# Performance work log

Hardware: AMD Instinct MI355X
Metric: run time of the kernel (lower is better)

## Reference

```python
import jax, jax.numpy as jnp
import numpy as np

B, T, D = 32, 2048, 256   # batch, encoder time steps, input_dim
H = 256                   # output_dim (GRU hidden)
A = 128                   # attention_dim
C = 4367                  # nb_classes
STEPS = 22                # max_out_t_steps


def setup_inputs() -> dict:
    key = jax.random.key(0)
    ks = jax.random.split(key, 11)
    s = 0.05
    return {
        "x": jax.random.normal(ks[0], (B, T, D), dtype=jnp.float32),
        # additive attention params: softmax_T(tanh(x Wx + h Wh) @ v)
        "Wx": jax.random.normal(ks[1], (D, A), dtype=jnp.float32) * s,
        "Wh": jax.random.normal(ks[2], (H, A), dtype=jnp.float32) * s,
        "v": jax.random.normal(ks[3], (A,), dtype=jnp.float32) * s,
        # torch GRUCell params
        "W_ih": jax.random.normal(ks[4], (3 * H, D), dtype=jnp.float32) * s,
        "W_hh": jax.random.normal(ks[5], (3 * H, H), dtype=jnp.float32) * s,
        "b_ih": jax.random.normal(ks[6], (3 * H,), dtype=jnp.float32) * s,
        "b_hh": jax.random.normal(ks[7], (3 * H,), dtype=jnp.float32) * s,
        # classifier
        "W_cls": jax.random.normal(ks[8], (C, H), dtype=jnp.float32) * s,
        "b_cls": jax.random.normal(ks[9], (C,), dtype=jnp.float32) * s,
    }


def reference(x, Wx, Wh, v, W_ih, W_hh, b_ih, b_hh, W_cls, b_cls):
    # dropout layers are identity in eval/reference mode
    xW = jnp.einsum("btd,da->bta", x, Wx)  # hoisted: constant across steps
    h0 = jnp.zeros((x.shape[0], H), dtype=x.dtype)

    def step(h, _):
        # additive attention over time axis
        e = jnp.einsum("bta,a->bt", jnp.tanh(xW + (h @ Wh)[:, None, :]), v)
        att = jax.nn.softmax(e, axis=1)          # [B, T]
        ctx = jnp.einsum("btd,bt->bd", x, att)   # weighted sum over T
        # torch GRUCell
        gi = ctx @ W_ih.T + b_ih                  # [B, 3H]
        gh = h @ W_hh.T + b_hh                    # [B, 3H]
        i_r, i_z, i_n = jnp.split(gi, 3, axis=1)
        h_r, h_z, h_n = jnp.split(gh, 3, axis=1)
        r = jax.nn.sigmoid(i_r + h_r)
        z = jax.nn.sigmoid(i_z + h_z)
        n = jnp.tanh(i_n + r * h_n)
        h_new = (1.0 - z) * n + z * h
        logits = h_new @ W_cls.T + b_cls          # [B, C]
        return h_new, logits

    _, outs = jax.lax.scan(step, h0, None, length=STEPS)  # [STEPS, B, C]
    return jnp.transpose(outs, (1, 0, 2))                 # [B, STEPS, C]
```

## Files before the change

kernel.cpp:

```cpp
#include <hip/hip_runtime.h>

#define BB 32
#define TT 2048
#define DD 256
#define HH 256
#define AA 128
#define CC 4367
#define CLS_LD 4480
#define NSTEPS 22
#define NCHUNK 32

typedef unsigned short ushortT;
typedef unsigned int uintT;
using frag8 = __attribute__((ext_vector_type(8))) short;
using f32x4 = __attribute__((ext_vector_type(4))) float;

__device__ __forceinline__ float tanh_fast(float u) {
  float e = __expf(2.0f * u);
  return 1.0f - 2.0f / (e + 1.0f);
}
__device__ __forceinline__ float sigmoid_fast(float u) {
  return 1.0f / (1.0f + __expf(-u));
}
__device__ __forceinline__ ushortT f2bf(float f) {
  unsigned int u = __float_as_uint(f);
  unsigned int r = (u + 0x7FFFu + ((u >> 16) & 1u)) >> 16;
  return (ushortT)r;
}
__device__ __forceinline__ float bf2f(ushortT v) {
  return __uint_as_float(((unsigned int)v) << 16);
}

__global__ __launch_bounds__(256) void trans_kernel(
    const float* __restrict__ Wx, const float* __restrict__ W_cls,
    float* __restrict__ WclsT, ushortT* __restrict__ WxT_bf) {
  int blk = blockIdx.x;
  __shared__ float tile[32][33];
  const int li = threadIdx.x >> 5, lj = threadIdx.x & 31;
  if (blk < 1096) {
    int i0 = (blk >> 3) * 32, j0 = (blk & 7) * 32;
#pragma unroll
    for (int k = 0; k < 4; ++k) {
      int i = i0 + li + k * 8;
      if (i < CC) tile[li + k * 8][lj] = W_cls[(size_t)i * 256 + j0 + lj];
    }
    __syncthreads();
#pragma unroll
    for (int k = 0; k < 4; ++k) {
      int j = j0 + li + k * 8, i = i0 + lj;
      if (i < CC) WclsT[(size_t)j * CLS_LD + i] = tile[lj][li + k * 8];
    }
  } else {
    blk -= 1096;
    int i0 = (blk >> 2) * 32, j0 = (blk & 3) * 32;
#pragma unroll
    for (int k = 0; k < 4; ++k)
      tile[li + k * 8][lj] = Wx[(size_t)(i0 + li + k * 8) * 128 + j0 + lj];
    __syncthreads();
#pragma unroll
    for (int k = 0; k < 4; ++k) {
      int j = j0 + li + k * 8;
      WxT_bf[(size_t)j * 256 + i0 + lj] = f2bf(tile[lj][li + k * 8]);
    }
  }
}

__global__ __launch_bounds__(256) void xw_mfma(
    const float* __restrict__ x, const ushortT* __restrict__ WxT_bf,
    ushortT* __restrict__ x_bf, ushortT* __restrict__ xWT) {
  __shared__ ushortT lds[2 * 128 * 72];
#define SX(r, c) lds[(r) * 72 + (c)]
#define SW(r, c) lds[128 * 72 + (r) * 72 + (c)]
#define ST(a, m) lds[(a) * 136 + (m)]
  const int tid = threadIdx.x;
  const int lane = tid & 63, w = tid >> 6;
  const int l15 = lane & 15, quad = lane >> 4;
  const int r0 = blockIdx.x * 128;
  const int bb = blockIdx.x >> 4, t0 = (blockIdx.x & 15) * 128;
  const int row = tid >> 1, half = tid & 1;

  f32x4 acc[2][8];
#pragma unroll
  for (int mt = 0; mt < 2; ++mt)
#pragma unroll
    for (int nt = 0; nt < 8; ++nt) acc[mt][nt] = (f32x4){0.f, 0.f, 0.f, 0.f};

  for (int kk0 = 0; kk0 < 256; kk0 += 64) {
    {
      const float4* xp = (const float4*)(x + (size_t)(r0 + row) * DD + kk0 + half * 32);
      uint4 pk[4];
#pragma unroll
      for (int i = 0; i < 4; ++i) {
        float4 f0 = xp[2 * i], f1 = xp[2 * i + 1];
        pk[i].x = (uintT)f2bf(f0.x) | ((uintT)f2bf(f0.y) << 16);
        pk[i].y = (uintT)f2bf(f0.z) | ((uintT)f2bf(f0.w) << 16);
        pk[i].z = (uintT)f2bf(f1.x) | ((uintT)f2bf(f1.y) << 16);
        pk[i].w = (uintT)f2bf(f1.z) | ((uintT)f2bf(f1.w) << 16);
      }
      uint4* sxp = (uint4*)&SX(row, half * 32);
      uint4* gxp = (uint4*)(x_bf + (size_t)(r0 + row) * DD + kk0 + half * 32);
#pragma unroll
      for (int i = 0; i < 4; ++i) { sxp[i] = pk[i]; gxp[i] = pk[i]; }
    }
    {
      const uint4* wp = (const uint4*)(WxT_bf + (size_t)row * DD + kk0 + half * 32);
      uint4* swp = (uint4*)&SW(row, half * 32);
#pragma unroll
      for (int i = 0; i < 4; ++i) swp[i] = wp[i];
    }
    __syncthreads();
#pragma unroll
    for (int kk = 0; kk < 2; ++kk) {
      frag8 a0 = *(const frag8*)&SX(w * 32 + l15, kk * 32 + quad * 8);
      frag8 a1 = *(const frag8*)&SX(w * 32 + 16 + l15, kk * 32 + quad * 8);
#pragma unroll
      for (int nt = 0; nt < 8; ++nt) {
        frag8 bf = *(const frag8*)&SW(nt * 16 + l15, kk * 32 + quad * 8);
        acc[0][nt] = __builtin_amdgcn_mfma_f32_16x16x32_bf16(a0, bf, acc[0][nt], 0, 0, 0);
        acc[1][nt] = __builtin_amdgcn_mfma_f32_16x16x32_bf16(a1, bf, acc[1][nt], 0, 0, 0);
      }
    }
    __syncthreads();
  }
#pragma unroll
  for (int mt = 0; mt < 2; ++mt)
#pragma unroll
    for (int nt = 0; nt < 8; ++nt)
#pragma unroll
      for (int r = 0; r < 4; ++r) {
        int m = w * 32 + mt * 16 + quad * 4 + r;
        int a = nt * 16 + l15;
        ST(a, m) = f2bf(acc[mt][nt][r]);
      }
  __syncthreads();
  {
    const uint4* sp = (const uint4*)&ST(row, half * 64);
    uint4* gp = (uint4*)(xWT + ((size_t)bb * AA + row) * TT + t0 + half * 64);
#pragma unroll
    for (int i = 0; i < 8; ++i) gp[i] = sp[i];
  }
#undef SX
#undef SW
#undef ST
}

__global__ __launch_bounds__(256) void gates_kernel(
    const float* __restrict__ ctx_part, const float* __restrict__ den_part,
    const float* __restrict__ hall, const float* __restrict__ W_ih,
    const float* __restrict__ W_hh, const float* __restrict__ b_ih,
    const float* __restrict__ b_hh, float* __restrict__ gi_buf,
    float* __restrict__ gh_buf, int s) {
  const int slice = blockIdx.x, b = blockIdx.y, tid = threadIdx.x;
  __shared__ __align__(16) float sctx[DD];
  __shared__ float sden;
  if (tid < 32) {
    float d = den_part[b * NCHUNK + tid];
#pragma unroll
    for (int off = 16; off > 0; off >>= 1) d += __shfl_down(d, off, 32);
    if (tid == 0) sden = d;
  }
  {
    float acc = 0.f;
#pragma unroll
    for (int c = 0; c < NCHUNK; ++c)
      acc += ctx_part[((size_t)b * NCHUNK + c) * DD + tid];
    sctx[tid] = acc;
  }
  __syncthreads();
  const float invd = 1.0f / sden;
  const int kq = tid & 15, gsub = tid >> 4;
  const float4* cp = (const float4*)sctx + kq * 4;
  const float4* hrow = (s >= 2) ? (const float4*)(hall + ((size_t)(s - 2) * BB + b) * HH) + kq * 4 : nullptr;
  float4 c4[4], h4[4];
#pragma unroll
  for (int j = 0; j < 4; ++j) {
    float4 cv = cp[j];
    c4[j].x = cv.x * invd; c4[j].y = cv.y * invd; c4[j].z = cv.z * invd; c4[j].w = cv.w * invd;
    if (hrow) h4[j] = hrow[j];
    else { h4[j].x = 0.f; h4[j].y = 0.f; h4[j].z = 0.f; h4[j].w = 0.f; }
  }
#pragma unroll
  for (int it = 0; it < 4; ++it) {
    const int g = slice * 64 + it * 16 + gsub;
    const float4* wi = (const float4*)(W_ih + (size_t)g * DD) + kq * 4;
    const float4* wh = (const float4*)(W_hh + (size_t)g * HH) + kq * 4;
    float gi = 0.f, gh = 0.f;
#pragma unroll
    for (int j = 0; j < 4; ++j) {
      float4 wv = wi[j];
      gi += c4[j].x * wv.x + c4[j].y * wv.y + c4[j].z * wv.z + c4[j].w * wv.w;
      wv = wh[j];
      gh += h4[j].x * wv.x + h4[j].y * wv.y + h4[j].z * wv.z + h4[j].w * wv.w;
    }
#pragma unroll
    for (int off = 8; off > 0; off >>= 1) {
      gi += __shfl_down(gi, off, 16);
      gh += __shfl_down(gh, off, 16);
    }
    if (kq == 0) {
      gi_buf[b * 768 + g] = gi + b_ih[g];
      gh_buf[b * 768 + g] = gh + b_hh[g];
    }
  }
}

__global__ __launch_bounds__(256) void hcomb_kernel(
    const float* __restrict__ gi_buf, const float* __restrict__ gh_buf,
    const float* __restrict__ Wh, float* __restrict__ hall,
    float* __restrict__ hWh_buf, int s) {
  const int b = blockIdx.x, as = blockIdx.y, i = threadIdx.x;
  __shared__ float sh[HH];
  __shared__ float part[8][32];
  {
    float gir = gi_buf[b * 768 + i], giz = gi_buf[b * 768 + 256 + i], gin = gi_buf[b * 768 + 512 + i];
    float ghr = gh_buf[b * 768 + i], ghz = gh_buf[b * 768 + 256 + i], ghn = gh_buf[b * 768 + 512 + i];
    float hp = (s >= 2) ? hall[((size_t)(s - 2) * BB + b) * HH + i] : 0.f;
    float r = sigmoid_fast(gir + ghr);
    float z = sigmoid_fast(giz + ghz);
    float n = tanh_fast(gin + r * ghn);
    float hv = (1.f - z) * n + z * hp;
    if (as == 0) hall[((size_t)(s - 1) * BB + b) * HH + i] = hv;
    sh[i] = hv;
  }
  __syncthreads();
  {
    const int a = i & 31, kq = i >> 5;
    const int ga = as * 32 + a;
    float acc = 0.f;
#pragma unroll
    for (int k = kq * 32; k < kq * 32 + 32; ++k)
      acc = fmaf(sh[k], Wh[k * AA + ga], acc);
    part[kq][a] = acc;
  }
  __syncthreads();
  if (i < 32) {
    float sum = part[0][i] + part[1][i] + part[2][i] + part[3][i]
              + part[4][i] + part[5][i] + part[6][i] + part[7][i];
    hWh_buf[b * AA + as * 32 + i] = sum;
  }
}

__global__ __launch_bounds__(256, 4) void att_kernel(
    const ushortT* __restrict__ x_bf, const ushortT* __restrict__ xWT_bf,
    const float* __restrict__ hWh_buf, const float* __restrict__ v,
    float* __restrict__ ctx_part, float* __restrict__ den_part) {
  const int tid = threadIdx.x;
  const int chunk = blockIdx.x;
  const int b = blockIdx.y;
  const int t0 = chunk * 64;
  __shared__ float sh_hWh[AA], sh_v[AA];
  __shared__ float sh_part[8 * 64];
  __shared__ float sh_w[64];
  __shared__ __align__(16) float sh_ctx[4 * DD];
  if (tid < AA) {
    sh_hWh[tid] = hWh_buf ? hWh_buf[b * AA + tid] : 0.f;
    sh_v[tid] = v[tid];
  }
  const int j4 = tid >> 6, dq = tid & 63;
  ushort4 xr[16];
  {
    const ushort4* xb4 = (const ushort4*)x_bf;
#pragma unroll
    for (int j = 0; j < 16; ++j)
      xr[j] = xb4[(((size_t)(b * TT + t0 + j * 4 + j4)) * DD >> 2) + dq];
  }
  __syncthreads();
  {
    const int q = tid >> 5, tp = tid & 31;
    float p0 = 0.f, p1 = 0.f;
    const ushort2* xw2 = (const ushort2*)xWT_bf;
    const size_t base = (size_t)b * (AA * TT / 2) + (t0 >> 1) + tp;
#pragma unroll
    for (int i = 0; i < 16; ++i) {
      int a = q * 16 + i;
      ushort2 u = xw2[base + (size_t)a * (TT / 2)];
      float hwa = sh_hWh[a], va = sh_v[a];
      p0 = fmaf(tanh_fast(bf2f(u.x) + hwa), va, p0);
      p1 = fmaf(tanh_fast(bf2f(u.y) + hwa), va, p1);
    }
    sh_part[q * 64 + 2 * tp] = p0;
    sh_part[q * 64 + 2 * tp + 1] = p1;
  }
  __syncthreads();
  if (tid < 64) {
    float e = 0.f;
#pragma unroll
    for (int q = 0; q < 8; ++q) e += sh_part[q * 64 + tid];
    sh_w[tid] = __expf(e);
  }
  __syncthreads();
  {
    float4 acc = {0.f, 0.f, 0.f, 0.f};
#pragma unroll
    for (int j = 0; j < 16; ++j) {
      float w = sh_w[j * 4 + j4];
      acc.x = fmaf(w, bf2f(xr[j].x), acc.x);
      acc.y = fmaf(w, bf2f(xr[j].y), acc.y);
      acc.z = fmaf(w, bf2f(xr[j].z), acc.z);
      acc.w = fmaf(w, bf2f(xr[j].w), acc.w);
    }
    ((float4*)sh_ctx)[j4 * 64 + dq] = acc;
  }
  __syncthreads();
  {
    float sum = sh_ctx[tid] + sh_ctx[DD + tid] + sh_ctx[2 * DD + tid] + sh_ctx[3 * DD + tid];
    ctx_part[((size_t)b * NCHUNK + chunk) * DD + tid] = sum;
  }
  if (tid < 64) {
    float ds = sh_w[tid];
#pragma unroll
    for (int off = 32; off > 0; off >>= 1) ds += __shfl_down(ds, off, 64);
    if (tid == 0) den_part[b * NCHUNK + chunk] = ds;
  }
}

__global__ __launch_bounds__(256) void cls_kernel(
    const float* __restrict__ hall, const float* __restrict__ WclsT,
    const float* __restrict__ b_cls, float* __restrict__ out) {
  const int tid = threadIdx.x;
  const int c0 = blockIdx.x * 128;
  const int r0 = blockIdx.y * 32;
  const int cq = tid & 31, rg = tid >> 5;
  const int c = c0 + cq * 4;
  __shared__ __align__(16) float shh[32 * HH];
  {
    const float4* hsrc = (const float4*)(hall + (size_t)r0 * HH);
    float4* hdst = (float4*)shh;
#pragma unroll
    for (int i = 0; i < 8; ++i) hdst[tid + 256 * i] = hsrc[tid + 256 * i];
  }
  __syncthreads();
  float acc[4][4];
#pragma unroll
  for (int j = 0; j < 4; ++j)
#pragma unroll
    for (int l = 0; l < 4; ++l) acc[j][l] = 0.f;
#pragma unroll 4
  for (int k = 0; k < HH; ++k) {
    float4 w4 = *(const float4*)(WclsT + (size_t)k * CLS_LD + c);
    float h0 = shh[(rg * 4 + 0) * HH + k];
    float h1 = shh[(rg * 4 + 1) * HH + k];
    float h2 = shh[(rg * 4 + 2) * HH + k];
    float h3 = shh[(rg * 4 + 3) * HH + k];
    acc[0][0] = fmaf(h0, w4.x, acc[0][0]); acc[0][1] = fmaf(h0, w4.y, acc[0][1]);
    acc[0][2] = fmaf(h0, w4.z, acc[0][2]); acc[0][3] = fmaf(h0, w4.w, acc[0][3]);
    acc[1][0] = fmaf(h1, w4.x, acc[1][0]); acc[1][1] = fmaf(h1, w4.y, acc[1][1]);
    acc[1][2] = fmaf(h1, w4.z, acc[1][2]); acc[1][3] = fmaf(h1, w4.w, acc[1][3]);
    acc[2][0] = fmaf(h2, w4.x, acc[2][0]); acc[2][1] = fmaf(h2, w4.y, acc[2][1]);
    acc[2][2] = fmaf(h2, w4.z, acc[2][2]); acc[2][3] = fmaf(h2, w4.w, acc[2][3]);
    acc[3][0] = fmaf(h3, w4.x, acc[3][0]); acc[3][1] = fmaf(h3, w4.y, acc[3][1]);
    acc[3][2] = fmaf(h3, w4.z, acc[3][2]); acc[3][3] = fmaf(h3, w4.w, acc[3][3]);
  }
#pragma unroll
  for (int j = 0; j < 4; ++j) {
    int row = r0 + rg * 4 + j;
    int bb = row & (BB - 1), st = row >> 5;
    size_t obase = ((size_t)bb * NSTEPS + st) * CC;
#pragma unroll
    for (int l = 0; l < 4; ++l) {
      int cc = c + l;
      if (cc < CC) out[obase + cc] = acc[j][l] + b_cls[cc];
    }
  }
}

extern "C" void kernel_launch(void* const* d_in, const int* in_sizes, int n_in,
                              void* d_out, int out_size, void* d_ws, size_t ws_size,
                              hipStream_t stream) {
  const float* x     = (const float*)d_in[0];
  const float* Wx    = (const float*)d_in[1];
  const float* Wh    = (const float*)d_in[2];
  const float* v     = (const float*)d_in[3];
  const float* W_ih  = (const float*)d_in[4];
  const float* W_hh  = (const float*)d_in[5];
  const float* b_ih  = (const float*)d_in[6];
  const float* b_hh  = (const float*)d_in[7];
  const float* W_cls = (const float*)d_in[8];
  const float* b_cls = (const float*)d_in[9];
  float* out = (float*)d_out;

  float* ctx_part = (float*)d_ws;
  float* den_part = ctx_part + (size_t)BB * NCHUNK * DD;
  float* hWh_buf  = den_part + BB * NCHUNK;
  float* gi_buf   = hWh_buf + BB * AA;
  float* gh_buf   = gi_buf + BB * 768;
  float* hall     = gh_buf + BB * 768;
  float* WclsT    = hall + (size_t)NSTEPS * BB * HH;
  ushortT* WxT_bf = (ushortT*)(WclsT + (size_t)256 * CLS_LD);
  ushortT* x_bf   = WxT_bf + 128 * 256;
  ushortT* xWT    = x_bf + (size_t)BB * TT * DD;

  trans_kernel<<<1096 + 32, 256, 0, stream>>>(Wx, W_cls, WclsT, WxT_bf);
  xw_mfma<<<(BB * TT) / 128, 256, 0, stream>>>(x, WxT_bf, x_bf, xWT);

  att_kernel<<<dim3(NCHUNK, BB), 256, 0, stream>>>(x_bf, xWT, nullptr, v, ctx_part, den_part);
  for (int s = 1; s < NSTEPS; ++s) {
    gates_kernel<<<dim3(12, BB), 256, 0, stream>>>(ctx_part, den_part, hall, W_ih, W_hh,
                                                   b_ih, b_hh, gi_buf, gh_buf, s);
    hcomb_kernel<<<dim3(BB, 4), 256, 0, stream>>>(gi_buf, gh_buf, Wh, hall, hWh_buf, s);
    att_kernel<<<dim3(NCHUNK, BB), 256, 0, stream>>>(x_bf, xWT, hWh_buf, v, ctx_part, den_part);
  }
  gates_kernel<<<dim3(12, BB), 256, 0, stream>>>(ctx_part, den_part, hall, W_ih, W_hh,
                                                 b_ih, b_hh, gi_buf, gh_buf, NSTEPS);
  hcomb_kernel<<<dim3(BB, 4), 256, 0, stream>>>(gi_buf, gh_buf, Wh, hall, hWh_buf, NSTEPS);
  cls_kernel<<<dim3(35, 22), 256, 0, stream>>>(hall, WclsT, b_cls, out);
}
```

Measured before the change: 722.6 us.

## Fuse GRU gates and state update into one kernel; tile classifier weights in LDS

Merges the gates and hcomb kernels into a single per-batch gru_kernel. Each thread computes full dot products for its hidden unit across the three gates, then applies the GRU update and the h@Wh projection in the same launch, which removes one launch and the gi/gh global round trip per step. The cost is far fewer blocks (32 instead of 384+128), and each thread walks a weight row serially with uncoalesced row-strided loads. The classifier kernel also now stages 32-row slabs of W_cls^T in shared memory and reads h as float4, cutting redundant global loads.

New measurement: 1.670 ms. +131.1%, slower.

```diff
diff --git a/kernel.cpp b/kernel.cpp
--- a/kernel.cpp
+++ b/kernel.cpp
@@ -7,6 +7,7 @@
 #define AA 128
 #define CC 4367
 #define CLS_LD 4480
+#define CLS_KP 32
 #define NSTEPS 22
 #define NCHUNK 32
 
@@ -144,14 +145,17 @@
 #undef ST
 }
 
-__global__ __launch_bounds__(256) void gates_kernel(
+__global__ __launch_bounds__(256) void gru_kernel(
     const float* __restrict__ ctx_part, const float* __restrict__ den_part,
-    const float* __restrict__ hall, const float* __restrict__ W_ih,
-    const float* __restrict__ W_hh, const float* __restrict__ b_ih,
-    const float* __restrict__ b_hh, float* __restrict__ gi_buf,
-    float* __restrict__ gh_buf, int s) {
-  const int slice = blockIdx.x, b = blockIdx.y, tid = threadIdx.x;
+    const float* __restrict__ W_ih, const float* __restrict__ W_hh,
+    const float* __restrict__ b_ih, const float* __restrict__ b_hh,
+    const float* __restrict__ Wh, float* __restrict__ hall,
+    float* __restrict__ hWh_buf, int s) {
+  const int b = blockIdx.x, tid = threadIdx.x;
   __shared__ __align__(16) float sctx[DD];
+  __shared__ __align__(16) float sh_prev[HH];
+  __shared__ __align__(16) float sh[HH];
+  __shared__ float part[2][AA];
   __shared__ float sden;
   if (tid < 32) {
     float d = den_part[b * NCHUNK + tid];
@@ -166,78 +170,55 @@
       acc += ctx_part[((size_t)b * NCHUNK + c) * DD + tid];
     sctx[tid] = acc;
   }
+  sh_prev[tid] = (s >= 2) ? hall[((size_t)(s - 2) * BB + b) * HH + tid] : 0.f;
   __syncthreads();
   const float invd = 1.0f / sden;
-  const int kq = tid & 15, gsub = tid >> 4;
-  const float4* cp = (const float4*)sctx + kq * 4;
-  const float4* hrow = (s >= 2) ? (const float4*)(hall + ((size_t)(s - 2) * BB + b) * HH) + kq * 4 : nullptr;
-  float4 c4[4], h4[4];
-#pragma unroll
-  for (int j = 0; j < 4; ++j) {
-    float4 cv = cp[j];
-    c4[j].x = cv.x * invd; c4[j].y = cv.y * invd; c4[j].z = cv.z * invd; c4[j].w = cv.w * invd;
-    if (hrow) h4[j] = hrow[j];
-    else { h4[j].x = 0.f; h4[j].y = 0.f; h4[j].z = 0.f; h4[j].w = 0.f; }
-  }
-#pragma unroll
-  for (int it = 0; it < 4; ++it) {
-    const int g = slice * 64 + it * 16 + gsub;
-    const float4* wi = (const float4*)(W_ih + (size_t)g * DD) + kq * 4;
-    const float4* wh = (const float4*)(W_hh + (size_t)g * HH) + kq * 4;
-    float gi = 0.f, gh = 0.f;
-#pragma unroll
-    for (int j = 0; j < 4; ++j) {
-      float4 wv = wi[j];
-      gi += c4[j].x * wv.x + c4[j].y * wv.y + c4[j].z * wv.z + c4[j].w * wv.w;
-      wv = wh[j];
-      gh += h4[j].x * wv.x + h4[j].y * wv.y + h4[j].z * wv.z + h4[j].w * wv.w;
-    }
-#pragma unroll
-    for (int off = 8; off > 0; off >>= 1) {
-      gi += __shfl_down(gi, off, 16);
-      gh += __shfl_down(gh, off, 16);
-    }
-    if (kq == 0) {
-      gi_buf[b * 768 + g] = gi + b_ih[g];
-      gh_buf[b * 768 + g] = gh + b_hh[g];
-    }
-  }
-}
-
-__global__ __launch_bounds__(256) void hcomb_kernel(
-    const float* __restrict__ gi_buf, const float* __restrict__ gh_buf,
-    const float* __restrict__ Wh, float* __restrict__ hall,
-    float* __restrict__ hWh_buf, int s) {
-  const int b = blockIdx.x, as = blockIdx.y, i = threadIdx.x;
-  __shared__ float sh[HH];
-  __shared__ float part[8][32];
-  {
-    float gir = gi_buf[b * 768 + i], giz = gi_buf[b * 768 + 256 + i], gin = gi_buf[b * 768 + 512 + i];
-    float ghr = gh_buf[b * 768 + i], ghz = gh_buf[b * 768 + 256 + i], ghn = gh_buf[b * 768 + 512 + i];
-    float hp = (s >= 2) ? hall[((size_t)(s - 2) * BB + b) * HH + i] : 0.f;
+  const float4* sctx4 = (const float4*)sctx;
+  const float4* shp4 = (const float4*)sh_prev;
+  float gi_g[3], gh_g[3];
+#pragma unroll
+  for (int gg = 0; gg < 3; ++gg) {
+    const float4* wi = (const float4*)(W_ih + (size_t)(gg * 256 + tid) * DD);
+    const float4* wh = (const float4*)(W_hh + (size_t)(gg * 256 + tid) * HH);
+    float ix = 0.f, iy = 0.f, iz = 0.f, iw = 0.f;
+    float hx = 0.f, hy = 0.f, hz = 0.f, hw = 0.f;
+#pragma unroll 8
+    for (int k4 = 0; k4 < DD / 4; ++k4) {
+      float4 wv = wi[k4], cv = sctx4[k4];
+      ix = fmaf(cv.x, wv.x, ix); iy = fmaf(cv.y, wv.y, iy);
+      iz = fmaf(cv.z, wv.z, iz); iw = fmaf(cv.w, wv.w, iw);
+      float4 wv2 = wh[k4], hv4 = shp4[k4];
+      hx = fmaf(hv4.x, wv2.x, hx); hy = fmaf(hv4.y, wv2.y, hy);
+      hz = fmaf(hv4.z, wv2.z, hz); hw = fmaf(hv4.w, wv2.w, hw);
+    }
+    gi_g[gg] = (ix + iy) + (iz + iw);
+    gh_g[gg] = (hx + hy) + (hz + hw);
+  }
+  {
+    float gir = gi_g[0] * invd + b_ih[tid];
+    float giz = gi_g[1] * invd + b_ih[256 + tid];
+    float gin = gi_g[2] * invd + b_ih[512 + tid];
+    float ghr = gh_g[0] + b_hh[tid];
+    float ghz = gh_g[1] + b_hh[256 + tid];
+    float ghn = gh_g[2] + b_hh[512 + tid];
     float r = sigmoid_fast(gir + ghr);
     float z = sigmoid_fast(giz + ghz);
     float n = tanh_fast(gin + r * ghn);
-    float hv = (1.f - z) * n + z * hp;
-    if (as == 0) hall[((size_t)(s - 1) * BB + b) * HH + i] = hv;
-    sh[i] = hv;
-  }
-  __syncthreads();
-  {
-    const int a = i & 31, kq = i >> 5;
-    const int ga = as * 32 + a;
+    float hv = (1.f - z) * n + z * sh_prev[tid];
+    hall[((size_t)(s - 1) * BB + b) * HH + tid] = hv;
+    sh[tid] = hv;
+  }
+  __syncthreads();
+  {
+    const int a = tid & 127, kh = tid >> 7;
     float acc = 0.f;
-#pragma unroll
-    for (int k = kq * 32; k < kq * 32 + 32; ++k)
-      acc = fmaf(sh[k], Wh[k * AA + ga], acc);
-    part[kq][a] = acc;
-  }
-  __syncthreads();
-  if (i < 32) {
-    float sum = part[0][i] + part[1][i] + part[2][i] + part[3][i]
-              + part[4][i] + part[5][i] + part[6][i] + part[7][i];
-    hWh_buf[b * AA + as * 32 + i] = sum;
-  }
+#pragma unroll 8
+    for (int k = kh * 128; k < kh * 128 + 128; ++k)
+      acc = fmaf(sh[k], Wh[k * AA + a], acc);
+    part[kh][a] = acc;
+  }
+  __syncthreads();
+  if (tid < AA) hWh_buf[b * AA + tid] = part[0][tid] + part[1][tid];
 }
 
 __global__ __launch_bounds__(256, 4) void att_kernel(
@@ -323,33 +304,49 @@
   const int cq = tid & 31, rg = tid >> 5;
   const int c = c0 + cq * 4;
   __shared__ __align__(16) float shh[32 * HH];
+  __shared__ __align__(16) float sW[CLS_KP][128];
   {
     const float4* hsrc = (const float4*)(hall + (size_t)r0 * HH);
     float4* hdst = (float4*)shh;
 #pragma unroll
     for (int i = 0; i < 8; ++i) hdst[tid + 256 * i] = hsrc[tid + 256 * i];
   }
-  __syncthreads();
   float acc[4][4];
 #pragma unroll
   for (int j = 0; j < 4; ++j)
 #pragma unroll
     for (int l = 0; l < 4; ++l) acc[j][l] = 0.f;
-#pragma unroll 4
-  for (int k = 0; k < HH; ++k) {
-    float4 w4 = *(const float4*)(WclsT + (size_t)k * CLS_LD + c);
-    float h0 = shh[(rg * 4 + 0) * HH + k];
-    float h1 = shh[(rg * 4 + 1) * HH + k];
-    float h2 = shh[(rg * 4 + 2) * HH + k];
-    float h3 = shh[(rg * 4 + 3) * HH + k];
-    acc[0][0] = fmaf(h0, w4.x, acc[0][0]); acc[0][1] = fmaf(h0, w4.y, acc[0][1]);
-    acc[0][2] = fmaf(h0, w4.z, acc[0][2]); acc[0][3] = fmaf(h0, w4.w, acc[0][3]);
-    acc[1][0] = fmaf(h1, w4.x, acc[1][0]); acc[1][1] = fmaf(h1, w4.y, acc[1][1]);
-    acc[1][2] = fmaf(h1, w4.z, acc[1][2]); acc[1][3] = fmaf(h1, w4.w, acc[1][3]);
-    acc[2][0] = fmaf(h2, w4.x, acc[2][0]); acc[2][1] = fmaf(h2, w4.y, acc[2][1]);
-    acc[2][2] = fmaf(h2, w4.z, acc[2][2]); acc[2][3] = fmaf(h2, w4.w, acc[2][3]);
-    acc[3][0] = fmaf(h3, w4.x, acc[3][0]); acc[3][1] = fmaf(h3, w4.y, acc[3][1]);
-    acc[3][2] = fmaf(h3, w4.z, acc[3][2]); acc[3][3] = fmaf(h3, w4.w, acc[3][3]);
+  for (int k0 = 0; k0 < HH; k0 += CLS_KP) {
+    __syncthreads();
+    {
+      const int tk = tid >> 5, tc = tid & 31;
+#pragma unroll
+      for (int kk = 0; kk < 4; ++kk) {
+        int k = tk * 4 + kk;
+        ((float4*)&sW[k][0])[tc] =
+            *(const float4*)(WclsT + (size_t)(k0 + k) * CLS_LD + c0 + tc * 4);
+      }
+    }
+    __syncthreads();
+#pragma unroll
+    for (int k4 = 0; k4 < CLS_KP / 4; ++k4) {
+      float4 w0 = ((const float4*)&sW[k4 * 4 + 0][0])[cq];
+      float4 w1 = ((const float4*)&sW[k4 * 4 + 1][0])[cq];
+      float4 w2 = ((const float4*)&sW[k4 * 4 + 2][0])[cq];
+      float4 w3 = ((const float4*)&sW[k4 * 4 + 3][0])[cq];
+#pragma unroll
+      for (int j = 0; j < 4; ++j) {
+        float4 h4v = *(const float4*)&shh[(rg * 4 + j) * HH + k0 + k4 * 4];
+        acc[j][0] = fmaf(h4v.x, w0.x, acc[j][0]); acc[j][1] = fmaf(h4v.x, w0.y, acc[j][1]);
+        acc[j][2] = fmaf(h4v.x, w0.z, acc[j][2]); acc[j][3] = fmaf(h4v.x, w0.w, acc[j][3]);
+        acc[j][0] = fmaf(h4v.y, w1.x, acc[j][0]); acc[j][1] = fmaf(h4v.y, w1.y, acc[j][1]);
+        acc[j][2] = fmaf(h4v.y, w1.z, acc[j][2]); acc[j][3] = fmaf(h4v.y, w1.w, acc[j][3]);
+        acc[j][0] = fmaf(h4v.z, w2.x, acc[j][0]); acc[j][1] = fmaf(h4v.z, w2.y, acc[j][1]);
+        acc[j][2] = fmaf(h4v.z, w2.z, acc[j][2]); acc[j][3] = fmaf(h4v.z, w2.w, acc[j][3]);
+        acc[j][0] = fmaf(h4v.w, w3.x, acc[j][0]); acc[j][1] = fmaf(h4v.w, w3.y, acc[j][1]);
+        acc[j][2] = fmaf(h4v.w, w3.z, acc[j][2]); acc[j][3] = fmaf(h4v.w, w3.w, acc[j][3]);
+      }
+    }
   }
 #pragma unroll
   for (int j = 0; j < 4; ++j) {
@@ -382,9 +379,7 @@
   float* ctx_part = (float*)d_ws;
   float* den_part = ctx_part + (size_t)BB * NCHUNK * DD;
   float* hWh_buf  = den_part + BB * NCHUNK;
-  float* gi_buf   = hWh_buf + BB * AA;
-  float* gh_buf   = gi_buf + BB * 768;
-  float* hall     = gh_buf + BB * 768;
+  float* hall     = hWh_buf + BB * AA;
   float* WclsT    = hall + (size_t)NSTEPS * BB * HH;
   ushortT* WxT_bf = (ushortT*)(WclsT + (size_t)256 * CLS_LD);
   ushortT* x_bf   = WxT_bf + 128 * 256;
@@ -395,13 +390,11 @@
 
   att_kernel<<<dim3(NCHUNK, BB), 256, 0, stream>>>(x_bf, xWT, nullptr, v, ctx_part, den_part);
   for (int s = 1; s < NSTEPS; ++s) {
-    gates_kernel<<<dim3(12, BB), 256, 0, stream>>>(ctx_part, den_part, hall, W_ih, W_hh,
-                                                   b_ih, b_hh, gi_buf, gh_buf, s);
-    hcomb_kernel<<<dim3(BB, 4), 256, 0, stream>>>(gi_buf, gh_buf, Wh, hall, hWh_buf, s);
+    gru_kernel<<<BB, 256, 0, stream>>>(ctx_part, den_part, W_ih, W_hh,
+                                       b_ih, b_hh, Wh, hall, hWh_buf, s);
     att_kernel<<<dim3(NCHUNK, BB), 256, 0, stream>>>(x_bf, xWT, hWh_buf, v, ctx_part, den_part);
   }
-  gates_kernel<<<dim3(12, BB), 256, 0, stream>>>(ctx_part, den_part, hall, W_ih, W_hh,
-                                                 b_ih, b_hh, gi_buf, gh_buf, NSTEPS);
-  hcomb_kernel<<<dim3(BB, 4), 256, 0, stream>>>(gi_buf, gh_buf, Wh, hall, hWh_buf, NSTEPS);
+  gru_kernel<<<BB, 256, 0, stream>>>(ctx_part, den_part, W_ih, W_hh,
+                                     b_ih, b_hh, Wh, hall, hWh_buf, NSTEPS);
   cls_kernel<<<dim3(35, 22), 256, 0, stream>>>(hall, WclsT, b_cls, out);
 }
```
